# Performance work log

Hardware: AMD Instinct MI355X
Metric: run time of the kernel (lower is better)

The kernel has to match this reference:

```python
import jax, jax.numpy as jnp
import numpy as np

N_NODES = 100000
N_EDGES = 1600000
IN_CH = 500
H1, C1 = 8, 8           # layer 1: 8 heads x 8 dims, concat -> 64
H2, C2 = 8, 3           # layer 2: 8 heads x 3 classes, mean over heads
NEG_SLOPE = 0.2         # PyG GATConv default


def gat_layer(x, src, dst, W, a_src, a_dst, b, concat):
    """PyG-style GATConv (self-loops already included in src/dst)."""
    N = x.shape[0]
    H, C = a_src.shape
    xw = (x @ W).reshape(N, H, C)                      # [N,H,C]
    al_src = jnp.einsum('nhc,hc->nh', xw, a_src)       # [N,H]
    al_dst = jnp.einsum('nhc,hc->nh', xw, a_dst)       # [N,H]
    e = jax.nn.leaky_relu(al_src[src] + al_dst[dst], NEG_SLOPE)  # [E,H]
    # segment softmax over incoming edges of each destination node
    m = jax.lax.stop_gradient(jax.ops.segment_max(e, dst, num_segments=N))
    ex = jnp.exp(e - m[dst])
    s = jax.ops.segment_sum(ex, dst, num_segments=N)
    alpha = ex / (s[dst] + 1e-16)                      # [E,H]
    out = jax.ops.segment_sum(alpha[:, :, None] * xw[src], dst, num_segments=N)  # [N,H,C]
    out = out.reshape(N, H * C) if concat else out.mean(axis=1)
    return out + b


def setup_inputs() -> dict:
    key = jax.random.key(0)
    ks = jax.random.split(key, 10)
    x = jax.random.normal(ks[0], (N_NODES, IN_CH), dtype=jnp.float32)
    edge_index = jax.random.randint(ks[1], (2, N_EDGES), 0, N_NODES, dtype=jnp.int64)
    sc1 = 1.0 / np.sqrt(IN_CH)
    sc2 = 1.0 / np.sqrt(H1 * C1)
    W1 = jax.random.normal(ks[2], (IN_CH, H1 * C1), dtype=jnp.float32) * sc1
    a1_src = jax.random.normal(ks[3], (H1, C1), dtype=jnp.float32) * 0.1
    a1_dst = jax.random.normal(ks[4], (H1, C1), dtype=jnp.float32) * 0.1
    b1 = jnp.zeros((H1 * C1,), dtype=jnp.float32)
    W2 = jax.random.normal(ks[5], (H1 * C1, H2 * C2), dtype=jnp.float32) * sc2
    a2_src = jax.random.normal(ks[6], (H2, C2), dtype=jnp.float32) * 0.1
    a2_dst = jax.random.normal(ks[7], (H2, C2), dtype=jnp.float32) * 0.1
    b2 = jnp.zeros((C2,), dtype=jnp.float32)
    return {"x": x, "W1": W1, "a1_src": a1_src, "a1_dst": a1_dst, "b1": b1,
            "W2": W2, "a2_src": a2_src, "a2_dst": a2_dst, "b2": b2,
            "edge_index": edge_index}


def reference(x, W1, a1_src, a1_dst, b1, W2, a2_src, a2_dst, b2, edge_index):
    N = x.shape[0]
    loop = jnp.arange(N, dtype=edge_index.dtype)   # PyG add_self_loops=True
    src = jnp.concatenate([edge_index[0], loop])
    dst = jnp.concatenate([edge_index[1], loop])
    h = jax.nn.elu(gat_layer(x, src, dst, W1, a1_src, a1_dst, b1, concat=True))
    out = gat_layer(h, src, dst, W2, a2_src, a2_dst, b2, concat=False)
    return jax.nn.softmax(out, axis=1)
```

## Files before the change

kernel.cpp:

```cpp
#include <hip/hip_runtime.h>
#include <math.h>

#define N_NODESC 100000
#define N_EDGESC 1600000
#define E_TOT    1700000
#define IN_CH    500
#define KPAD     512
#define D1 64
#define D2 24
#define D2P 32
#define NBKT 391
#define CAP  5120
#define EPB  4096
#define NPB  416
#define GEMB 3125

typedef __attribute__((ext_vector_type(8))) short short8;
typedef __attribute__((ext_vector_type(4))) float f32x4;

__device__ inline short f2bf(float f) {
    unsigned u = __float_as_uint(f);
    u += 0x7fffu + ((u >> 16) & 1u);
    return (short)(u >> 16);
}
__device__ inline unsigned pkbf(float a, float b) {
    const unsigned ua = __float_as_uint(a) + 0x8000u;
    const unsigned ub = __float_as_uint(b) + 0x8000u;
    return __builtin_amdgcn_perm(ub, ua, 0x07060302u);
}
__device__ inline float bflo(unsigned u) { return __uint_as_float(u << 16); }
__device__ inline float bfhi(unsigned u) { return __uint_as_float(u & 0xffff0000u); }

__global__ __launch_bounds__(256) void k_init(int* __restrict__ gcnt,
                                              const float* __restrict__ W1,
                                              short* __restrict__ wT) {
    const int tid = blockIdx.x * 256 + threadIdx.x;
    for (int i = tid; i < D1 * KPAD; i += 16384) {
        const int n = i >> 9, k = i & (KPAD - 1);
        wT[i] = (k < IN_CH) ? f2bf(W1[k * D1 + n]) : (short)0;
    }
    for (int i = tid; i < NBKT * 32; i += 16384) gcnt[i] = 0;
}

__global__ __launch_bounds__(256) void k_pg(const int* __restrict__ ei,
                                            int* __restrict__ gcnt,
                                            int* __restrict__ tmp,
                                            const float* __restrict__ x,
                                            const short* __restrict__ wT,
                                            const float* __restrict__ a1s,
                                            const float* __restrict__ a1d,
                                            short* __restrict__ xw1b,
                                            float* __restrict__ al1s,
                                            float* __restrict__ al1d) {
    __shared__ short xs[32 * 520];
    const int t = threadIdx.x;

    if (blockIdx.x < NPB) {
        int* hist  = (int*)xs;
        int* lbase = hist + NBKT;
        const int e0 = blockIdx.x * EPB;
        for (int i = t; i < NBKT; i += 256) hist[i] = 0;
        __syncthreads();
        int se[16], de[16], mo[16];
#pragma unroll
        for (int i = 0; i < 16; i++) {
            const int e = e0 + i * 256 + t;
            int s = -1, d = 0;
            if (e < E_TOT) {
                if (e < N_EDGESC) { s = ei[e]; d = ei[N_EDGESC + e]; }
                else { s = d = e - N_EDGESC; }
            }
            se[i] = s; de[i] = d;
            mo[i] = (s >= 0) ? atomicAdd(&hist[d >> 8], 1) : 0;
        }
        __syncthreads();
        for (int i = t; i < NBKT; i += 256)
            lbase[i] = hist[i] ? (i * CAP + atomicAdd(&gcnt[i * 32], hist[i])) : 0;
        __syncthreads();
#pragma unroll
        for (int i = 0; i < 16; i++) {
            if (se[i] >= 0) {
                const int b = de[i] >> 8;
                const int idx = lbase[b] + mo[i];
                if (idx < (b + 1) * CAP)
                    tmp[idx] = se[i] | ((de[i] & 255) << 17);
            }
        }
        return;
    }

    const int rowBase = (blockIdx.x - NPB) * 32;
    const int r = t >> 3, j = t & 7;
    const float* xr = x + (long)(rowBase + r) * IN_CH;
    short* xrow = xs + r * 520;
#pragma unroll
    for (int i = 0; i < 16; i++) {
        const int c = j + i * 8;
        if (c < 125) {
            const float4 v = *(const float4*)(xr + c * 4);
            const unsigned lo = pkbf(v.x, v.y);
            const unsigned hi = pkbf(v.z, v.w);
            *(uint2*)(xrow + c * 4) = make_uint2(lo, hi);
        }
    }
    if (j < 6) *(unsigned*)(xrow + 500 + j * 2) = 0u;
    __syncthreads();

    const int lane = t & 63, wv = t >> 6;
    const int m = lane & 15, kg = lane >> 4;
    f32x4 acc[2];
    acc[0] = (f32x4){0.f, 0.f, 0.f, 0.f};
    acc[1] = (f32x4){0.f, 0.f, 0.f, 0.f};
    const short* wcol = wT + (wv * 16 + m) * KPAD;
#pragma unroll
    for (int k0 = 0; k0 < KPAD; k0 += 32) {
        const short8 bf = *(const short8*)(wcol + k0 + kg * 8);
#pragma unroll
        for (int mf = 0; mf < 2; mf++) {
            const short8 af = *(const short8*)(xs + (mf * 16 + m) * 520 + k0 + kg * 8);
            acc[mf] = __builtin_amdgcn_mfma_f32_16x16x32_bf16(af, bf, acc[mf], 0, 0, 0);
        }
    }
    const int col = wv * 16 + m;
    const float as = a1s[col];
    const float ad = a1d[col];
    const int hh = wv * 2 + (m >> 3);
#pragma unroll
    for (int mf = 0; mf < 2; mf++) {
#pragma unroll
        for (int jj = 0; jj < 4; jj++) {
            const int row = rowBase + mf * 16 + kg * 4 + jj;
            const float v = acc[mf][jj];
            xw1b[(long)row * D1 + col] = f2bf(v);
            float ts = v * as, td = v * ad;
            ts += __shfl_xor(ts, 1, 64); td += __shfl_xor(td, 1, 64);
            ts += __shfl_xor(ts, 2, 64); td += __shfl_xor(td, 2, 64);
            ts += __shfl_xor(ts, 4, 64); td += __shfl_xor(td, 4, 64);
            if ((m & 7) == 0) {
                al1s[row * 8 + hh] = ts;
                al1d[row * 8 + hh] = td;
            }
        }
    }
}

__global__ __launch_bounds__(512) void k_bucket2(const int* __restrict__ gcnt,
                                                 const int* __restrict__ tmp,
                                                 int* __restrict__ off,
                                                 int* __restrict__ srt) {
    __shared__ int se[CAP];
    __shared__ int cnts[256];
    __shared__ int sc[256];
    __shared__ int lcur[256];
    __shared__ int red[8];
    __shared__ int sbase;
    const int b = blockIdx.x;
    const int t = threadIdx.x;
    const int cnt = min(gcnt[b * 32], CAP);

    int pre = (t < b) ? min(gcnt[t * 32], CAP) : 0;
#pragma unroll
    for (int m = 1; m < 64; m <<= 1) pre += __shfl_xor(pre, m, 64);
    if ((t & 63) == 0) red[t >> 6] = pre;
    if (t < 256) cnts[t] = 0;
    __syncthreads();
    if (t == 0) {
        int sb = 0;
#pragma unroll
        for (int i = 0; i < 8; i++) sb += red[i];
        sbase = sb;
    }
    __syncthreads();
    const int base = sbase;

    for (int i = t; i < cnt; i += 512) {
        const int p = tmp[b * CAP + i];
        se[i] = p;
        atomicAdd(&cnts[p >> 17], 1);
    }
    __syncthreads();
    if (t < 256) sc[t] = cnts[t];
    __syncthreads();
    for (int d = 1; d < 256; d <<= 1) {
        const int u = (t >= d && t < 256) ? sc[t - d] : 0;
        __syncthreads();
        if (t < 256) sc[t] += u;
        __syncthreads();
    }
    const int nodeBase = b << 8;
    const int nNodes = min(256, N_NODESC - nodeBase);
    if (t < 256) {
        const int excl = base + sc[t] - cnts[t];
        if (t < nNodes) off[nodeBase + t] = excl;
        lcur[t] = excl;
    }
    if (b == 0 && t == 0) off[N_NODESC] = E_TOT;
    __syncthreads();
    for (int i = t; i < cnt; i += 512) {
        const int p = se[i];
        const int pos = atomicAdd(&lcur[p >> 17], 1);
        srt[pos] = p & 0x1FFFF;
    }
}

__global__ __launch_bounds__(256) void k_gat1(const int* __restrict__ off,
                                              const int* __restrict__ srt_src,
                                              const float* __restrict__ al1s,
                                              const float* __restrict__ al1d,
                                              const short* __restrict__ xw1b,
                                              const float* __restrict__ b1,
                                              const float* __restrict__ W2,
                                              const float* __restrict__ a2s,
                                              const float* __restrict__ a2d,
                                              float* __restrict__ xw2,
                                              float* __restrict__ al2d) {
    __shared__ float w2s[D1 * D2];
    __shared__ float hrow[4][D1];
    const int tid = threadIdx.x;
    for (int i = tid; i < D1 * D2; i += 256) w2s[i] = W2[i];
    __syncthreads();

    const int lane = tid & 63;
    const int wid = tid >> 6;
    const int n = blockIdx.x * 4 + wid;
    const int e8 = lane >> 3;
    const int hd = lane & 7;

    const float ald = al1d[n * 8 + hd];
    const int kend = off[n + 1];

    float4 a0 = make_float4(0.f, 0.f, 0.f, 0.f);
    float4 a1 = make_float4(0.f, 0.f, 0.f, 0.f);
    float ssum = 0.f;
    int k = off[n] + e8;
    int s = (k < kend) ? srt_src[k] : -1;
    float al = 0.f;
    uint4 v = make_uint4(0u, 0u, 0u, 0u);
    if (s >= 0) {
        al = al1s[s * 8 + hd];
        v = *(const uint4*)(xw1b + (long)s * D1 + hd * 8);
    }
    while (s >= 0) {
        const int kn = k + 8;
        const int sn = (kn < kend) ? srt_src[kn] : -1;
        float aln = 0.f;
        uint4 vn = v;
        if (sn >= 0) {
            aln = al1s[sn * 8 + hd];
            vn = *(const uint4*)(xw1b + (long)sn * D1 + hd * 8);
        }
        float ev = al + ald;
        ev = ev > 0.f ? ev : 0.2f * ev;
        const float ex = __expf(ev);
        a0.x += ex * bflo(v.x); a0.y += ex * bfhi(v.x);
        a0.z += ex * bflo(v.y); a0.w += ex * bfhi(v.y);
        a1.x += ex * bflo(v.z); a1.y += ex * bfhi(v.z);
        a1.z += ex * bflo(v.w); a1.w += ex * bfhi(v.w);
        ssum += ex;
        k = kn; s = sn; al = aln; v = vn;
    }
#pragma unroll
    for (int mm = 8; mm < 64; mm <<= 1) {
        a0.x += __shfl_xor(a0.x, mm, 64); a0.y += __shfl_xor(a0.y, mm, 64);
        a0.z += __shfl_xor(a0.z, mm, 64); a0.w += __shfl_xor(a0.w, mm, 64);
        a1.x += __shfl_xor(a1.x, mm, 64); a1.y += __shfl_xor(a1.y, mm, 64);
        a1.z += __shfl_xor(a1.z, mm, 64); a1.w += __shfl_xor(a1.w, mm, 64);
        ssum  += __shfl_xor(ssum,  mm, 64);
    }
    const float inv = 1.0f / (ssum + 1e-16f);
    const float4 bb0 = *(const float4*)(b1 + hd * 8);
    const float4 bb1 = *(const float4*)(b1 + hd * 8 + 4);
    float4 r0, r1;
    r0.x = a0.x * inv + bb0.x; r0.x = r0.x > 0.f ? r0.x : expm1f(r0.x);
    r0.y = a0.y * inv + bb0.y; r0.y = r0.y > 0.f ? r0.y : expm1f(r0.y);
    r0.z = a0.z * inv + bb0.z; r0.z = r0.z > 0.f ? r0.z : expm1f(r0.z);
    r0.w = a0.w * inv + bb0.w; r0.w = r0.w > 0.f ? r0.w : expm1f(r0.w);
    r1.x = a1.x * inv + bb1.x; r1.x = r1.x > 0.f ? r1.x : expm1f(r1.x);
    r1.y = a1.y * inv + bb1.y; r1.y = r1.y > 0.f ? r1.y : expm1f(r1.y);
    r1.z = a1.z * inv + bb1.z; r1.z = r1.z > 0.f ? r1.z : expm1f(r1.z);
    r1.w = a1.w * inv + bb1.w; r1.w = r1.w > 0.f ? r1.w : expm1f(r1.w);
    if (e8 == 0) {
        *(float4*)(&hrow[wid][hd * 8])     = r0;
        *(float4*)(&hrow[wid][hd * 8 + 4]) = r1;
    }
    const int half = lane / 24;
    const int j2 = lane - half * 24;
    const int cb = (half == 1) ? 32 : 0;
    float o = 0.f;
#pragma unroll
    for (int c4 = 0; c4 < 8; c4++) {
        const float4 hv = *(const float4*)(&hrow[wid][cb + c4 * 4]);
        const float* wr = w2s + (cb + c4 * 4) * D2 + j2;
        o += hv.x * wr[0] + hv.y * wr[D2] + hv.z * wr[2 * D2] + hv.w * wr[3 * D2];
    }
    const int src2 = (lane < 24) ? lane + 24 : lane;
    o += __shfl(o, src2, 64);
    if (lane < 24) {
        const int h3 = j2 / 3;
        xw2[(long)n * D2P + h3 * 4 + (j2 - 3 * h3)] = o;
    }
    const float ps = o * a2s[j2];
    const float pd = o * a2d[j2];
    const int hb = 3 * (lane & 7);
    const float s3 = __shfl(ps, hb, 64) + __shfl(ps, hb + 1, 64) + __shfl(ps, hb + 2, 64);
    const float d3 = __shfl(pd, hb, 64) + __shfl(pd, hb + 1, 64) + __shfl(pd, hb + 2, 64);
    if (lane < 8) {
        xw2[(long)n * D2P + lane * 4 + 3] = s3;
        al2d[n * 8 + lane] = d3;
    }
}

__global__ __launch_bounds__(256) void k_gat2(const int* __restrict__ off,
                                              const int* __restrict__ srt_src,
                                              const float* __restrict__ al2d,
                                              const float* __restrict__ xw2,
                                              const float* __restrict__ b2,
                                              float* __restrict__ out) {
    const int tid = threadIdx.x;
    const int lane = tid & 63;
    const int wid = tid >> 6;
    const int n = blockIdx.x * 4 + wid;
    const int e8 = lane >> 3;
    const int hd = lane & 7;

    const float ald = al2d[n * 8 + hd];
    const int kend = off[n + 1];

    float ax = 0.f, ay = 0.f, az = 0.f, ssum = 0.f;
    int k = off[n] + e8;
    int s = (k < kend) ? srt_src[k] : -1;
    float4 v = make_float4(0.f, 0.f, 0.f, 0.f);
    if (s >= 0) v = *(const float4*)(xw2 + (long)s * D2P + hd * 4);
    while (s >= 0) {
        const int kn = k + 8;
        const int sn = (kn < kend) ? srt_src[kn] : -1;
        float4 vn = v;
        if (sn >= 0) vn = *(const float4*)(xw2 + (long)sn * D2P + hd * 4);
        float ev = v.w + ald;
        ev = ev > 0.f ? ev : 0.2f * ev;
        const float ex = __expf(ev);
        ax += ex * v.x; ay += ex * v.y; az += ex * v.z;
        ssum += ex;
        k = kn; s = sn; v = vn;
    }
#pragma unroll
    for (int mm = 8; mm < 64; mm <<= 1) {
        ax += __shfl_xor(ax, mm, 64);
        ay += __shfl_xor(ay, mm, 64);
        az += __shfl_xor(az, mm, 64);
        ssum += __shfl_xor(ssum, mm, 64);
    }
    const float inv = 1.0f / (ssum + 1e-16f);
    float mx = ax * inv, my = ay * inv, mz = az * inv;
#pragma unroll
    for (int mm = 1; mm < 8; mm <<= 1) {
        mx += __shfl_xor(mx, mm, 64);
        my += __shfl_xor(my, mm, 64);
        mz += __shfl_xor(mz, mm, 64);
    }
    const float l0 = mx * 0.125f + b2[0];
    const float l1 = my * 0.125f + b2[1];
    const float l2 = mz * 0.125f + b2[2];
    const float mmax = fmaxf(l0, fmaxf(l1, l2));
    const float ee0 = expf(l0 - mmax), ee1 = expf(l1 - mmax), ee2 = expf(l2 - mmax);
    const float dinv = 1.0f / (ee0 + ee1 + ee2);
    if (lane < 3) {
        const float p = (lane == 0) ? ee0 : (lane == 1) ? ee1 : ee2;
        out[(long)n * 3 + lane] = p * dinv;
    }
}

extern "C" void kernel_launch(void* const* d_in, const int* in_sizes, int n_in,
                              void* d_out, int out_size, void* d_ws, size_t ws_size,
                              hipStream_t stream) {
    const float* x   = (const float*)d_in[0];
    const float* W1  = (const float*)d_in[1];
    const float* a1s = (const float*)d_in[2];
    const float* a1d = (const float*)d_in[3];
    const float* b1  = (const float*)d_in[4];
    const float* W2  = (const float*)d_in[5];
    const float* a2s = (const float*)d_in[6];
    const float* a2d = (const float*)d_in[7];
    const float* b2  = (const float*)d_in[8];
    const int*   ei  = (const int*)d_in[9];
    float* out = (float*)d_out;

    float* ws   = (float*)d_ws;
    float* xw2  = ws;
    float* al1s = xw2  + 3200000;
    float* al1d = al1s + 800000;
    float* al2d = al1d + 800000;
    short* xw1b = (short*)(al2d + 800000);
    int* off    = (int*)(xw1b + 6400000);
    int* gcnt   = off + 100004;
    int* srt    = gcnt + NBKT * 32;
    short* wT   = (short*)(srt + 1700000);
    int* tmp    = (int*)xw2;

    k_init<<<64, 256, 0, stream>>>(gcnt, W1, wT);
    k_pg<<<NPB + GEMB, 256, 0, stream>>>(ei, gcnt, tmp, x, wT, a1s, a1d,
                                         xw1b, al1s, al1d);
    k_bucket2<<<NBKT, 512, 0, stream>>>(gcnt, tmp, off, srt);
    k_gat1<<<N_NODESC / 4, 256, 0, stream>>>(off, srt, al1s, al1d, xw1b, b1,
                                             W2, a2s, a2d, xw2, al2d);
    k_gat2<<<N_NODESC / 4, 256, 0, stream>>>(off, srt, al2d, xw2, b2, out);
}
```

Before: 467.0 us.

## Use one block per node in GAT aggregation kernels and store layer-2 features as fp16

Both aggregation kernels now assign a full 256-thread block (32 edge slots) to each destination node instead of one wave per node, with a shared-memory cross-wave reduction before the epilogue. The manual next-edge prefetch is dropped in favour of a simple strided loop. Layer-2 projected features and source logits are stored as half precision to halve gather bytes, and the workspace layout is reshuffled so the temp buffer no longer aliases xw2. With about 17 edges per node on average, most of the 32 slots idle, and the extra syncthreads and shared reduction add overhead. Block count also grows fourfold.

Measured after the change: 630.2 us. 1.35x slower.

```diff
diff --git a/kernel.cpp b/kernel.cpp
--- a/kernel.cpp
+++ b/kernel.cpp
@@ -1,4 +1,5 @@
 #include <hip/hip_runtime.h>
+#include <hip/hip_fp16.h>
 #include <math.h>
 
 #define N_NODESC 100000
@@ -212,19 +213,18 @@
                                               const float* __restrict__ W2,
                                               const float* __restrict__ a2s,
                                               const float* __restrict__ a2d,
-                                              float* __restrict__ xw2,
+                                              __half* __restrict__ xw2h,
                                               float* __restrict__ al2d) {
     __shared__ float w2s[D1 * D2];
-    __shared__ float hrow[4][D1];
-    const int tid = threadIdx.x;
-    for (int i = tid; i < D1 * D2; i += 256) w2s[i] = W2[i];
-    __syncthreads();
-
-    const int lane = tid & 63;
-    const int wid = tid >> 6;
-    const int n = blockIdx.x * 4 + wid;
-    const int e8 = lane >> 3;
-    const int hd = lane & 7;
+    __shared__ float part[3][8][10];
+    __shared__ float hrow[D1];
+    const int t = threadIdx.x;
+    for (int i = t; i < D1 * D2; i += 256) w2s[i] = W2[i];
+
+    const int n = blockIdx.x;
+    const int lane = t & 63, w = t >> 6;
+    const int slot = t >> 3;
+    const int hd = t & 7;
 
     const float ald = al1d[n * 8 + hd];
     const int kend = off[n + 1];
@@ -232,23 +232,10 @@
     float4 a0 = make_float4(0.f, 0.f, 0.f, 0.f);
     float4 a1 = make_float4(0.f, 0.f, 0.f, 0.f);
     float ssum = 0.f;
-    int k = off[n] + e8;
-    int s = (k < kend) ? srt_src[k] : -1;
-    float al = 0.f;
-    uint4 v = make_uint4(0u, 0u, 0u, 0u);
-    if (s >= 0) {
-        al = al1s[s * 8 + hd];
-        v = *(const uint4*)(xw1b + (long)s * D1 + hd * 8);
-    }
-    while (s >= 0) {
-        const int kn = k + 8;
-        const int sn = (kn < kend) ? srt_src[kn] : -1;
-        float aln = 0.f;
-        uint4 vn = v;
-        if (sn >= 0) {
-            aln = al1s[sn * 8 + hd];
-            vn = *(const uint4*)(xw1b + (long)sn * D1 + hd * 8);
-        }
+    for (int k = off[n] + slot; k < kend; k += 32) {
+        const int s = srt_src[k];
+        const float al = al1s[s * 8 + hd];
+        const uint4 v = *(const uint4*)(xw1b + (long)s * D1 + hd * 8);
         float ev = al + ald;
         ev = ev > 0.f ? ev : 0.2f * ev;
         const float ex = __expf(ev);
@@ -257,7 +244,6 @@
         a1.x += ex * bflo(v.z); a1.y += ex * bfhi(v.z);
         a1.z += ex * bflo(v.w); a1.w += ex * bfhi(v.w);
         ssum += ex;
-        k = kn; s = sn; al = aln; v = vn;
     }
 #pragma unroll
     for (int mm = 8; mm < 64; mm <<= 1) {
@@ -267,81 +253,101 @@
         a1.z += __shfl_xor(a1.z, mm, 64); a1.w += __shfl_xor(a1.w, mm, 64);
         ssum  += __shfl_xor(ssum,  mm, 64);
     }
-    const float inv = 1.0f / (ssum + 1e-16f);
-    const float4 bb0 = *(const float4*)(b1 + hd * 8);
-    const float4 bb1 = *(const float4*)(b1 + hd * 8 + 4);
-    float4 r0, r1;
-    r0.x = a0.x * inv + bb0.x; r0.x = r0.x > 0.f ? r0.x : expm1f(r0.x);
-    r0.y = a0.y * inv + bb0.y; r0.y = r0.y > 0.f ? r0.y : expm1f(r0.y);
-    r0.z = a0.z * inv + bb0.z; r0.z = r0.z > 0.f ? r0.z : expm1f(r0.z);
-    r0.w = a0.w * inv + bb0.w; r0.w = r0.w > 0.f ? r0.w : expm1f(r0.w);
-    r1.x = a1.x * inv + bb1.x; r1.x = r1.x > 0.f ? r1.x : expm1f(r1.x);
-    r1.y = a1.y * inv + bb1.y; r1.y = r1.y > 0.f ? r1.y : expm1f(r1.y);
-    r1.z = a1.z * inv + bb1.z; r1.z = r1.z > 0.f ? r1.z : expm1f(r1.z);
-    r1.w = a1.w * inv + bb1.w; r1.w = r1.w > 0.f ? r1.w : expm1f(r1.w);
-    if (e8 == 0) {
-        *(float4*)(&hrow[wid][hd * 8])     = r0;
-        *(float4*)(&hrow[wid][hd * 8 + 4]) = r1;
-    }
-    const int half = lane / 24;
-    const int j2 = lane - half * 24;
-    const int cb = (half == 1) ? 32 : 0;
-    float o = 0.f;
-#pragma unroll
-    for (int c4 = 0; c4 < 8; c4++) {
-        const float4 hv = *(const float4*)(&hrow[wid][cb + c4 * 4]);
-        const float* wr = w2s + (cb + c4 * 4) * D2 + j2;
-        o += hv.x * wr[0] + hv.y * wr[D2] + hv.z * wr[2 * D2] + hv.w * wr[3 * D2];
-    }
-    const int src2 = (lane < 24) ? lane + 24 : lane;
-    o += __shfl(o, src2, 64);
-    if (lane < 24) {
-        const int h3 = j2 / 3;
-        xw2[(long)n * D2P + h3 * 4 + (j2 - 3 * h3)] = o;
-    }
-    const float ps = o * a2s[j2];
-    const float pd = o * a2d[j2];
-    const int hb = 3 * (lane & 7);
-    const float s3 = __shfl(ps, hb, 64) + __shfl(ps, hb + 1, 64) + __shfl(ps, hb + 2, 64);
-    const float d3 = __shfl(pd, hb, 64) + __shfl(pd, hb + 1, 64) + __shfl(pd, hb + 2, 64);
-    if (lane < 8) {
-        xw2[(long)n * D2P + lane * 4 + 3] = s3;
-        al2d[n * 8 + lane] = d3;
+    if (w > 0 && lane < 8) {
+        float* p = &part[w - 1][lane][0];
+        p[0] = a0.x; p[1] = a0.y; p[2] = a0.z; p[3] = a0.w;
+        p[4] = a1.x; p[5] = a1.y; p[6] = a1.z; p[7] = a1.w;
+        p[8] = ssum;
+    }
+    __syncthreads();
+    if (w == 0) {
+        float p9[9];
+        if (lane < 8) {
+            p9[0] = a0.x; p9[1] = a0.y; p9[2] = a0.z; p9[3] = a0.w;
+            p9[4] = a1.x; p9[5] = a1.y; p9[6] = a1.z; p9[7] = a1.w;
+            p9[8] = ssum;
+        } else if (lane < 32) {
+            const float* p = &part[(lane >> 3) - 1][lane & 7][0];
+#pragma unroll
+            for (int j = 0; j < 9; j++) p9[j] = p[j];
+        } else {
+#pragma unroll
+            for (int j = 0; j < 9; j++) p9[j] = 0.f;
+        }
+#pragma unroll
+        for (int mm = 8; mm < 32; mm <<= 1)
+#pragma unroll
+            for (int j = 0; j < 9; j++) p9[j] += __shfl_xor(p9[j], mm, 64);
+        if (lane < 8) {
+            const float inv = 1.0f / (p9[8] + 1e-16f);
+            const float4 bb0 = *(const float4*)(b1 + lane * 8);
+            const float4 bb1 = *(const float4*)(b1 + lane * 8 + 4);
+            float r[8];
+            r[0] = p9[0] * inv + bb0.x; r[1] = p9[1] * inv + bb0.y;
+            r[2] = p9[2] * inv + bb0.z; r[3] = p9[3] * inv + bb0.w;
+            r[4] = p9[4] * inv + bb1.x; r[5] = p9[5] * inv + bb1.y;
+            r[6] = p9[6] * inv + bb1.z; r[7] = p9[7] * inv + bb1.w;
+#pragma unroll
+            for (int i = 0; i < 8; i++) {
+                r[i] = r[i] > 0.f ? r[i] : expm1f(r[i]);
+                hrow[lane * 8 + i] = r[i];
+            }
+        }
+        const int half_ = lane / 24;
+        const int j2 = lane - half_ * 24;
+        const int cb = (half_ == 1) ? 32 : 0;
+        float o = 0.f;
+#pragma unroll
+        for (int c4 = 0; c4 < 8; c4++) {
+            const float4 hv = *(const float4*)(&hrow[cb + c4 * 4]);
+            const float* wr = w2s + (cb + c4 * 4) * D2 + j2;
+            o += hv.x * wr[0] + hv.y * wr[D2] + hv.z * wr[2 * D2] + hv.w * wr[3 * D2];
+        }
+        const int src2 = (lane < 24) ? lane + 24 : lane;
+        o += __shfl(o, src2, 64);
+        if (lane < 24) {
+            const int h3 = j2 / 3;
+            xw2h[(long)n * D2P + h3 * 4 + (j2 - 3 * h3)] = __float2half(o);
+        }
+        const float ps = o * a2s[j2];
+        const float pd = o * a2d[j2];
+        const int hb = 3 * (lane & 7);
+        const float s3 = __shfl(ps, hb, 64) + __shfl(ps, hb + 1, 64) + __shfl(ps, hb + 2, 64);
+        const float d3 = __shfl(pd, hb, 64) + __shfl(pd, hb + 1, 64) + __shfl(pd, hb + 2, 64);
+        if (lane < 8) {
+            xw2h[(long)n * D2P + lane * 4 + 3] = __float2half(s3);
+            al2d[n * 8 + lane] = d3;
+        }
     }
 }
 
 __global__ __launch_bounds__(256) void k_gat2(const int* __restrict__ off,
                                               const int* __restrict__ srt_src,
                                               const float* __restrict__ al2d,
-                                              const float* __restrict__ xw2,
+                                              const __half* __restrict__ xw2h,
                                               const float* __restrict__ b2,
                                               float* __restrict__ out) {
-    const int tid = threadIdx.x;
-    const int lane = tid & 63;
-    const int wid = tid >> 6;
-    const int n = blockIdx.x * 4 + wid;
-    const int e8 = lane >> 3;
-    const int hd = lane & 7;
+    __shared__ float part[3][8][5];
+    const int t = threadIdx.x;
+    const int n = blockIdx.x;
+    const int lane = t & 63, w = t >> 6;
+    const int slot = t >> 3;
+    const int hd = t & 7;
 
     const float ald = al2d[n * 8 + hd];
     const int kend = off[n + 1];
 
     float ax = 0.f, ay = 0.f, az = 0.f, ssum = 0.f;
-    int k = off[n] + e8;
-    int s = (k < kend) ? srt_src[k] : -1;
-    float4 v = make_float4(0.f, 0.f, 0.f, 0.f);
-    if (s >= 0) v = *(const float4*)(xw2 + (long)s * D2P + hd * 4);
-    while (s >= 0) {
-        const int kn = k + 8;
-        const int sn = (kn < kend) ? srt_src[kn] : -1;
-        float4 vn = v;
-        if (sn >= 0) vn = *(const float4*)(xw2 + (long)sn * D2P + hd * 4);
-        float ev = v.w + ald;
+    for (int k = off[n] + slot; k < kend; k += 32) {
+        const int s = srt_src[k];
+        const __half2* hp = (const __half2*)(xw2h + (long)s * D2P + hd * 4);
+        const float2 f0 = __half22float2(hp[0]);
+        const float2 f1 = __half22float2(hp[1]);
+        float ev = f1.y + ald;
         ev = ev > 0.f ? ev : 0.2f * ev;
         const float ex = __expf(ev);
-        ax += ex * v.x; ay += ex * v.y; az += ex * v.z;
+        ax += ex * f0.x; ay += ex * f0.y; az += ex * f1.x;
         ssum += ex;
-        k = kn; s = sn; v = vn;
     }
 #pragma unroll
     for (int mm = 8; mm < 64; mm <<= 1) {
@@ -350,23 +356,44 @@
         az += __shfl_xor(az, mm, 64);
         ssum += __shfl_xor(ssum, mm, 64);
     }
-    const float inv = 1.0f / (ssum + 1e-16f);
-    float mx = ax * inv, my = ay * inv, mz = az * inv;
-#pragma unroll
-    for (int mm = 1; mm < 8; mm <<= 1) {
-        mx += __shfl_xor(mx, mm, 64);
-        my += __shfl_xor(my, mm, 64);
-        mz += __shfl_xor(mz, mm, 64);
-    }
-    const float l0 = mx * 0.125f + b2[0];
-    const float l1 = my * 0.125f + b2[1];
-    const float l2 = mz * 0.125f + b2[2];
-    const float mmax = fmaxf(l0, fmaxf(l1, l2));
-    const float ee0 = expf(l0 - mmax), ee1 = expf(l1 - mmax), ee2 = expf(l2 - mmax);
-    const float dinv = 1.0f / (ee0 + ee1 + ee2);
-    if (lane < 3) {
-        const float p = (lane == 0) ? ee0 : (lane == 1) ? ee1 : ee2;
-        out[(long)n * 3 + lane] = p * dinv;
+    if (w > 0 && lane < 8) {
+        float* p = &part[w - 1][lane][0];
+        p[0] = ax; p[1] = ay; p[2] = az; p[3] = ssum;
+    }
+    __syncthreads();
+    if (w == 0) {
+        float p4[4];
+        if (lane < 8) { p4[0] = ax; p4[1] = ay; p4[2] = az; p4[3] = ssum; }
+        else if (lane < 32) {
+            const float* p = &part[(lane >> 3) - 1][lane & 7][0];
+#pragma unroll
+            for (int j = 0; j < 4; j++) p4[j] = p[j];
+        } else {
+#pragma unroll
+            for (int j = 0; j < 4; j++) p4[j] = 0.f;
+        }
+#pragma unroll
+        for (int mm = 8; mm < 32; mm <<= 1)
+#pragma unroll
+            for (int j = 0; j < 4; j++) p4[j] += __shfl_xor(p4[j], mm, 64);
+        const float inv = 1.0f / (p4[3] + 1e-16f);
+        float mx = p4[0] * inv, my = p4[1] * inv, mz = p4[2] * inv;
+#pragma unroll
+        for (int mm = 1; mm < 8; mm <<= 1) {
+            mx += __shfl_xor(mx, mm, 64);
+            my += __shfl_xor(my, mm, 64);
+            mz += __shfl_xor(mz, mm, 64);
+        }
+        const float l0 = mx * 0.125f + b2[0];
+        const float l1 = my * 0.125f + b2[1];
+        const float l2 = mz * 0.125f + b2[2];
+        const float mmax = fmaxf(l0, fmaxf(l1, l2));
+        const float ee0 = expf(l0 - mmax), ee1 = expf(l1 - mmax), ee2 = expf(l2 - mmax);
+        const float dinv = 1.0f / (ee0 + ee1 + ee2);
+        if (lane < 3) {
+            const float p = (lane == 0) ? ee0 : (lane == 1) ? ee1 : ee2;
+            out[(long)n * 3 + lane] = p * dinv;
+        }
     }
 }
 
@@ -385,23 +412,23 @@
     const int*   ei  = (const int*)d_in[9];
     float* out = (float*)d_out;
 
-    float* ws   = (float*)d_ws;
-    float* xw2  = ws;
-    float* al1s = xw2  + 3200000;
-    float* al1d = al1s + 800000;
-    float* al2d = al1d + 800000;
-    short* xw1b = (short*)(al2d + 800000);
-    int* off    = (int*)(xw1b + 6400000);
-    int* gcnt   = off + 100004;
-    int* srt    = gcnt + NBKT * 32;
-    short* wT   = (short*)(srt + 1700000);
-    int* tmp    = (int*)xw2;
+    float* ws    = (float*)d_ws;
+    float* al1s  = ws;
+    float* al1d  = al1s + 800000;
+    float* al2d  = al1d + 800000;
+    short* xw1b  = (short*)(al2d + 800000);
+    __half* xw2h = (__half*)(xw1b + 6400000);
+    int* off     = (int*)(xw2h + 3200000);
+    int* gcnt    = off + 100004;
+    int* srt     = gcnt + NBKT * 32;
+    short* wT    = (short*)(srt + 1700000);
+    int* tmp     = (int*)(wT + 32768);
 
     k_init<<<64, 256, 0, stream>>>(gcnt, W1, wT);
     k_pg<<<NPB + GEMB, 256, 0, stream>>>(ei, gcnt, tmp, x, wT, a1s, a1d,
                                          xw1b, al1s, al1d);
     k_bucket2<<<NBKT, 512, 0, stream>>>(gcnt, tmp, off, srt);
-    k_gat1<<<N_NODESC / 4, 256, 0, stream>>>(off, srt, al1s, al1d, xw1b, b1,
-                                             W2, a2s, a2d, xw2, al2d);
-    k_gat2<<<N_NODESC / 4, 256, 0, stream>>>(off, srt, al2d, xw2, b2, out);
-}
+    k_gat1<<<N_NODESC, 256, 0, stream>>>(off, srt, al1s, al1d, xw1b, b1,
+                                         W2, a2s, a2d, xw2h, al2d);
+    k_gat2<<<N_NODESC, 256, 0, stream>>>(off, srt, al2d, xw2h, b2, out);
+}
```
